# Performance work log

Measured on AMD Instinct MI355X. Metric: run time of the kernel, lower is better.

The kernel has to match this reference:

```python
import jax, jax.numpy as jnp
import numpy as np

NUM_HEADS = 8
NEG_LARGE = -1e9  # stands in for -inf under the causal mask; masked entries get exactly 0 entmax weight


def _entmax15(z):
    """Exact 1.5-entmax along the last axis (Peters & Martins 2019 sort-based algorithm)."""
    z = z * 0.5
    zs = -jnp.sort(-z, axis=-1)                      # descending sort
    T = z.shape[-1]
    k = jnp.arange(1, T + 1, dtype=z.dtype)
    mean = jnp.cumsum(zs, axis=-1) / k
    mean_sq = jnp.cumsum(zs * zs, axis=-1) / k
    ss = k * (mean_sq - mean * mean)
    delta = (1.0 - ss) / k
    tau = mean - jnp.sqrt(jnp.maximum(delta, 0.0))
    support = jnp.sum(tau <= zs, axis=-1, keepdims=True)      # support size >= 1
    tau_star = jnp.take_along_axis(tau, support - 1, axis=-1)
    return jnp.square(jnp.maximum(z - tau_star, 0.0))


def setup_inputs() -> dict:
    key = jax.random.key(0)
    ks = jax.random.split(key, 9)
    B, T, D, H = 2, 2048, 512, NUM_HEADS
    dk = D // H
    s = 1.0 / np.sqrt(D)
    so = 1.0 / np.sqrt(dk)
    x = jax.random.normal(ks[0], (B, T, D), jnp.float32)
    Wq = jax.random.uniform(ks[1], (D, D), jnp.float32, -s, s)
    bq = jax.random.uniform(ks[2], (D,), jnp.float32, -s, s)
    Wk = jax.random.uniform(ks[3], (D, D), jnp.float32, -s, s)
    bk = jax.random.uniform(ks[4], (D,), jnp.float32, -s, s)
    Wv = jax.random.uniform(ks[5], (D, D), jnp.float32, -s, s)
    bv = jax.random.uniform(ks[6], (D,), jnp.float32, -s, s)
    Wo = jax.random.uniform(ks[7], (dk, D), jnp.float32, -so, so)
    bo = jax.random.uniform(ks[8], (D,), jnp.float32, -so, so)
    return {"x": x, "Wq": Wq, "bq": bq, "Wk": Wk, "bk": bk, "Wv": Wv, "bv": bv, "Wo": Wo, "bo": bo}


def reference(x, Wq, bq, Wk, bk, Wv, bv, Wo, bo):
    B, T, D = x.shape
    H = NUM_HEADS
    dk = D // H
    Q = (x @ Wq + bq).reshape(B, T, H, dk).transpose(0, 2, 1, 3)   # [B,H,T,dk]
    K = (x @ Wk + bk).reshape(B, T, H, dk).transpose(0, 2, 1, 3)
    V = (x @ Wv + bv).reshape(B, T, H, dk).transpose(0, 2, 1, 3)
    scores = jnp.einsum('bhtd,bhsd->bhts', Q, K) / np.float32(np.sqrt(dk))
    causal = jnp.triu(jnp.ones((T, T), bool), k=1)                 # True above diagonal
    scores = jnp.where(causal[None, None, :, :], jnp.float32(NEG_LARGE), scores)
    weights = _entmax15(scores)                                    # [B,H,T,T]
    weights_avg = weights.mean(axis=1)                             # [B,T,T]
    V_combined = V.mean(axis=1)                                    # [B,T,dk]
    out = jnp.einsum('bts,bsd->btd', weights_avg, V_combined)      # [B,T,dk]
    return out @ Wo + bo, weights_avg
```

## Files before the change

kernel.cpp:

```cpp
#include <hip/hip_runtime.h>
#include <hip/hip_bf16.h>
#include <cstdint>

#define B_ 2
#define T_ 2048
#define D_ 512
#define H_ 8
#define DK_ 64
#define TQ_ 4
#define NTL_ (T_ / TQ_)
#define M_ (B_ * T_)

#define SSC_ 8192.0f
#define S2_  (SSC_ * SSC_)

__global__ __launch_bounds__(256) void gemm_bias_kernel(
    const float* __restrict__ A, const float* __restrict__ W,
    const float* __restrict__ bias, float* __restrict__ C,
    int M, int N, int K)
{
  __shared__ float As[32][68];
  __shared__ float Bs[32][68];
  const int bm = blockIdx.y * 64;
  const int bn = blockIdx.x * 64;
  const int tid = threadIdx.x;
  const int tx = tid & 15, ty = tid >> 4;
  float acc[4][4] = {};
  for (int k0 = 0; k0 < K; k0 += 32) {
    {
      const int r = tid >> 2;
      const int c = (tid & 3) << 2;
      const float4 a0 = *reinterpret_cast<const float4*>(&A[(size_t)(bm + r) * K + k0 + c]);
      const float4 a1 = *reinterpret_cast<const float4*>(&A[(size_t)(bm + r) * K + k0 + 16 + c]);
      As[c + 0][r] = a0.x;  As[c + 1][r] = a0.y;  As[c + 2][r] = a0.z;  As[c + 3][r] = a0.w;
      As[c + 16][r] = a1.x; As[c + 17][r] = a1.y; As[c + 18][r] = a1.z; As[c + 19][r] = a1.w;
    }
    {
      const int r = tid >> 4;
      const int c = (tid & 15) << 2;
      *reinterpret_cast<float4*>(&Bs[r][c]) =
          *reinterpret_cast<const float4*>(&W[(size_t)(k0 + r) * N + bn + c]);
      *reinterpret_cast<float4*>(&Bs[r + 16][c]) =
          *reinterpret_cast<const float4*>(&W[(size_t)(k0 + 16 + r) * N + bn + c]);
    }
    __syncthreads();
#pragma unroll
    for (int kk = 0; kk < 32; ++kk) {
      const float4 av = *reinterpret_cast<const float4*>(&As[kk][ty * 4]);
      const float4 bv = *reinterpret_cast<const float4*>(&Bs[kk][tx * 4]);
      acc[0][0] = fmaf(av.x, bv.x, acc[0][0]); acc[0][1] = fmaf(av.x, bv.y, acc[0][1]);
      acc[0][2] = fmaf(av.x, bv.z, acc[0][2]); acc[0][3] = fmaf(av.x, bv.w, acc[0][3]);
      acc[1][0] = fmaf(av.y, bv.x, acc[1][0]); acc[1][1] = fmaf(av.y, bv.y, acc[1][1]);
      acc[1][2] = fmaf(av.y, bv.z, acc[1][2]); acc[1][3] = fmaf(av.y, bv.w, acc[1][3]);
      acc[2][0] = fmaf(av.z, bv.x, acc[2][0]); acc[2][1] = fmaf(av.z, bv.y, acc[2][1]);
      acc[2][2] = fmaf(av.z, bv.z, acc[2][2]); acc[2][3] = fmaf(av.z, bv.w, acc[2][3]);
      acc[3][0] = fmaf(av.w, bv.x, acc[3][0]); acc[3][1] = fmaf(av.w, bv.y, acc[3][1]);
      acc[3][2] = fmaf(av.w, bv.z, acc[3][2]); acc[3][3] = fmaf(av.w, bv.w, acc[3][3]);
    }
    __syncthreads();
  }
#pragma unroll
  for (int i = 0; i < 4; ++i) {
    const int row = bm + ty * 4 + i;
#pragma unroll
    for (int j = 0; j < 4; ++j) {
      const int col = bn + tx * 4 + j;
      C[(size_t)row * N + col] = acc[i][j] + bias[col];
    }
  }
}

__global__ __launch_bounds__(256) void gemm_bias_kernelT(
    const float* __restrict__ A, const float* __restrict__ W,
    const float* __restrict__ bias, float* __restrict__ Ct,
    int M, int N, int K)
{
  __shared__ float As[32][68];
  __shared__ float Bs[32][68];
  const int bm = blockIdx.y * 64;
  const int bn = blockIdx.x * 64;
  const int tid = threadIdx.x;
  const int tx = tid & 15, ty = tid >> 4;
  float acc[4][4] = {};
  for (int k0 = 0; k0 < K; k0 += 32) {
    {
      const int r = tid >> 2;
      const int c = (tid & 3) << 2;
      const float4 a0 = *reinterpret_cast<const float4*>(&A[(size_t)(bm + r) * K + k0 + c]);
      const float4 a1 = *reinterpret_cast<const float4*>(&A[(size_t)(bm + r) * K + k0 + 16 + c]);
      As[c + 0][r] = a0.x;  As[c + 1][r] = a0.y;  As[c + 2][r] = a0.z;  As[c + 3][r] = a0.w;
      As[c + 16][r] = a1.x; As[c + 17][r] = a1.y; As[c + 18][r] = a1.z; As[c + 19][r] = a1.w;
    }
    {
      const int r = tid >> 4;
      const int c = (tid & 15) << 2;
      *reinterpret_cast<float4*>(&Bs[r][c]) =
          *reinterpret_cast<const float4*>(&W[(size_t)(k0 + r) * N + bn + c]);
      *reinterpret_cast<float4*>(&Bs[r + 16][c]) =
          *reinterpret_cast<const float4*>(&W[(size_t)(k0 + 16 + r) * N + bn + c]);
    }
    __syncthreads();
#pragma unroll
    for (int kk = 0; kk < 32; ++kk) {
      const float4 av = *reinterpret_cast<const float4*>(&As[kk][ty * 4]);
      const float4 bv = *reinterpret_cast<const float4*>(&Bs[kk][tx * 4]);
      acc[0][0] = fmaf(av.x, bv.x, acc[0][0]); acc[0][1] = fmaf(av.x, bv.y, acc[0][1]);
      acc[0][2] = fmaf(av.x, bv.z, acc[0][2]); acc[0][3] = fmaf(av.x, bv.w, acc[0][3]);
      acc[1][0] = fmaf(av.y, bv.x, acc[1][0]); acc[1][1] = fmaf(av.y, bv.y, acc[1][1]);
      acc[1][2] = fmaf(av.y, bv.z, acc[1][2]); acc[1][3] = fmaf(av.y, bv.w, acc[1][3]);
      acc[2][0] = fmaf(av.z, bv.x, acc[2][0]); acc[2][1] = fmaf(av.z, bv.y, acc[2][1]);
      acc[2][2] = fmaf(av.z, bv.z, acc[2][2]); acc[2][3] = fmaf(av.z, bv.w, acc[2][3]);
      acc[3][0] = fmaf(av.w, bv.x, acc[3][0]); acc[3][1] = fmaf(av.w, bv.y, acc[3][1]);
      acc[3][2] = fmaf(av.w, bv.z, acc[3][2]); acc[3][3] = fmaf(av.w, bv.w, acc[3][3]);
    }
    __syncthreads();
  }
#pragma unroll
  for (int j = 0; j < 4; ++j) {
    const int col = bn + tx * 4 + j;
    const float bb = bias[col];
    const float4 v = make_float4(acc[0][j] + bb, acc[1][j] + bb, acc[2][j] + bb, acc[3][j] + bb);
    *reinterpret_cast<float4*>(&Ct[(size_t)col * M + bm + ty * 4]) = v;
  }
}

__global__ __launch_bounds__(256) void vcombine_kernel(const float* __restrict__ V,
                                                       float* __restrict__ Vc)
{
  const int idx = blockIdx.x * 256 + threadIdx.x;
  if (idx >= M_ * DK_) return;
  const int row = idx >> 6, d = idx & 63;
  float s = 0.f;
#pragma unroll
  for (int h = 0; h < H_; ++h) s += V[(size_t)row * D_ + h * DK_ + d];
  Vc[idx] = s * 0.125f;
}

__global__ __launch_bounds__(256) void zero_kernel(float4* __restrict__ p, int n4)
{
  const int stride = gridDim.x * 256;
  const float4 z = make_float4(0.f, 0.f, 0.f, 0.f);
  for (int i = blockIdx.x * 256 + threadIdx.x; i < n4; i += stride) p[i] = z;
}

__global__ __launch_bounds__(256, 6)
void attn_kernel(
    const float* __restrict__ Qg, const float* __restrict__ Kt,
    float* __restrict__ wavg)
{
  __shared__ short ssc[TQ_][T_];

  const int tid = threadIdx.x;
  const int bid = blockIdx.x;
  const int h = bid >> 10;
  const int b = (bid >> 9) & 1;
  const int tile = (NTL_ - 1) - (bid & 511);
  const int t0 = tile * TQ_;
  const int nS = t0 + TQ_;
  const int wave = __builtin_amdgcn_readfirstlane(tid >> 6);
  const int lane = tid & 63;

  {
    const float* Qp = &Qg[(size_t)(b * T_ + t0) * D_ + h * DK_];
#pragma unroll 1
    for (int c = 0; c < T_; c += 1024) {
      if (c < nS) {
        const int s0 = min(tid * 4 + c, nS - 4);
        const float* Ktp = &Kt[(size_t)(h * DK_) * M_ + b * T_ + s0];
        float4 a[TQ_];
#pragma unroll
        for (int r = 0; r < TQ_; ++r) a[r] = make_float4(0.f, 0.f, 0.f, 0.f);
#pragma unroll 2
        for (int d4 = 0; d4 < 16; ++d4) {
          const float4 k0 = *reinterpret_cast<const float4*>(Ktp + (size_t)(d4 * 4 + 0) * M_);
          const float4 k1 = *reinterpret_cast<const float4*>(Ktp + (size_t)(d4 * 4 + 1) * M_);
          const float4 k2 = *reinterpret_cast<const float4*>(Ktp + (size_t)(d4 * 4 + 2) * M_);
          const float4 k3 = *reinterpret_cast<const float4*>(Ktp + (size_t)(d4 * 4 + 3) * M_);
#pragma unroll
          for (int r = 0; r < TQ_; ++r) {
            const float q0 = Qp[r * D_ + d4 * 4 + 0];
            const float q1 = Qp[r * D_ + d4 * 4 + 1];
            const float q2 = Qp[r * D_ + d4 * 4 + 2];
            const float q3 = Qp[r * D_ + d4 * 4 + 3];
            a[r].x = fmaf(q0, k0.x, a[r].x); a[r].y = fmaf(q0, k0.y, a[r].y);
            a[r].z = fmaf(q0, k0.z, a[r].z); a[r].w = fmaf(q0, k0.w, a[r].w);
            a[r].x = fmaf(q1, k1.x, a[r].x); a[r].y = fmaf(q1, k1.y, a[r].y);
            a[r].z = fmaf(q1, k1.z, a[r].z); a[r].w = fmaf(q1, k1.w, a[r].w);
            a[r].x = fmaf(q2, k2.x, a[r].x); a[r].y = fmaf(q2, k2.y, a[r].y);
            a[r].z = fmaf(q2, k2.z, a[r].z); a[r].w = fmaf(q2, k2.w, a[r].w);
            a[r].x = fmaf(q3, k3.x, a[r].x); a[r].y = fmaf(q3, k3.y, a[r].y);
            a[r].z = fmaf(q3, k3.z, a[r].z); a[r].w = fmaf(q3, k3.w, a[r].w);
          }
        }
#pragma unroll
        for (int r = 0; r < TQ_; ++r) {
          const int i0 = __float2int_rn(fminf(fmaxf(a[r].x * 512.f, -32000.f), 32000.f));
          const int i1 = __float2int_rn(fminf(fmaxf(a[r].y * 512.f, -32000.f), 32000.f));
          const int i2 = __float2int_rn(fminf(fmaxf(a[r].z * 512.f, -32000.f), 32000.f));
          const int i3 = __float2int_rn(fminf(fmaxf(a[r].w * 512.f, -32000.f), 32000.f));
          short4 st; st.x = (short)i0; st.y = (short)i1; st.z = (short)i2; st.w = (short)i3;
          *reinterpret_cast<short4*>(&ssc[r][s0]) = st;
        }
      }
    }
  }
  __syncthreads();

  const int t = t0 + wave;
  const int n = t + 1;
  float srow[32];

#pragma unroll
  for (int j = 0; j < 4; ++j) {
    if (j * 512 < n) {
      const uint4 pk = *reinterpret_cast<const uint4*>(&ssc[wave][j * 512 + lane * 8]);
      const unsigned pw[4] = {pk.x, pk.y, pk.z, pk.w};
#pragma unroll
      for (int q = 0; q < 4; ++q) {
        const int s_lo = j * 512 + lane * 8 + q * 2;
        const float lo = (float)((int)(short)(pw[q] & 0xffffu));
        const float hi = (float)((int)pw[q] >> 16);
        srow[j * 8 + q * 2 + 0] = (s_lo + 0 < n) ? lo : -1e30f;
        srow[j * 8 + q * 2 + 1] = (s_lo + 1 < n) ? hi : -1e30f;
      }
    } else {
#pragma unroll
      for (int q = 0; q < 8; ++q) srow[j * 8 + q] = -1e30f;
    }
  }
  asm volatile("" ::: "memory");

  float mx = -1e30f;
#pragma unroll
  for (int i = 0; i < 32; ++i) mx = fmaxf(mx, srow[i]);
#pragma unroll
  for (int m = 32; m >= 1; m >>= 1) mx = fmaxf(mx, __shfl_xor(mx, m, 64));

  float tau = mx - SSC_;
#pragma unroll 1
  for (int it = 0; it < 12; ++it) {
    float s1 = 0.f, s2 = 0.f, cn = 0.f;
#pragma unroll
    for (int j = 0; j < 4; ++j) {
      if (j * 512 < n) {
#pragma unroll
        for (int q = 0; q < 8; ++q) {
          const float u = fmaxf(srow[j * 8 + q] - tau, 0.f);
          s1 += u;
          s2 = fmaf(u, u, s2);
          cn += (u > 0.f) ? 1.f : 0.f;
        }
      }
    }
#pragma unroll
    for (int m = 32; m >= 1; m >>= 1) {
      s1 += __shfl_xor(s1, m, 64);
      s2 += __shfl_xor(s2, m, 64);
    }
    if (fabsf(s2 - S2_) < 672.f) break;
    if (it < 3) {
#pragma unroll
      for (int m = 32; m >= 1; m >>= 1) cn += __shfl_xor(cn, m, 64);
      const float kf = fmaxf(cn, 1.f);
      const float mu = tau + s1 / kf;
      const float ss = s2 - s1 * s1 / kf;
      tau = mu - sqrtf(fmaxf((S2_ - ss) / kf, 0.f));
    } else {
      tau += (s2 - S2_) / fmaxf(2.f * s1, 1e-6f);
    }
  }
  tau = fminf(tau, mx - 1.f);

  const float wconv = 0.125f / (SSC_ * SSC_);
  float* const wrow = &wavg[(size_t)(b * T_ + t) * T_];
#pragma unroll
  for (int j = 0; j < 4; ++j) {
    if (j * 512 < n) {
#pragma unroll
      for (int q = 0; q < 8; ++q) {
        const float u = fmaxf(srow[j * 8 + q] - tau, 0.f);
        if (__any(u > 0.f)) {
          if (u > 0.f) {
            const int s = j * 512 + lane * 8 + q;
            atomicAdd(&wrow[s], u * u * wconv);
          }
        }
      }
    }
  }
}

__global__ __launch_bounds__(256) void pv_kernel(
    const float* __restrict__ wavg, const float* __restrict__ Vc,
    float* __restrict__ AO)
{
  __shared__ float part[4][TQ_][DK_];
  const int tid = threadIdx.x;
  const int m0 = blockIdx.x * TQ_;
  const int b = m0 >> 11;
  const int tl = m0 & (T_ - 1);
  const int wave = __builtin_amdgcn_readfirstlane(tid >> 6);
  const int lane = tid & 63;

  const int smax = min((wave + 1) * 512, tl + TQ_);
  float a0 = 0.f, a1 = 0.f, a2 = 0.f, a3 = 0.f;
  const float* w0 = &wavg[(size_t)(m0 + 0) * T_];
  const float* w1 = &wavg[(size_t)(m0 + 1) * T_];
  const float* w2 = &wavg[(size_t)(m0 + 2) * T_];
  const float* w3 = &wavg[(size_t)(m0 + 3) * T_];
#pragma unroll 1
  for (int s = wave * 512; s < smax; ++s) {
    const float v = Vc[(size_t)(b * T_ + s) * DK_ + lane];
    a0 = fmaf(w0[s], v, a0);
    a1 = fmaf(w1[s], v, a1);
    a2 = fmaf(w2[s], v, a2);
    a3 = fmaf(w3[s], v, a3);
  }
  part[wave][0][lane] = a0;
  part[wave][1][lane] = a1;
  part[wave][2][lane] = a2;
  part[wave][3][lane] = a3;
  __syncthreads();
  {
    const int r = wave;
    const float o = part[0][r][lane] + part[1][r][lane] +
                    part[2][r][lane] + part[3][r][lane];
    AO[(size_t)(m0 + r) * DK_ + lane] = o;
  }
}

extern "C" void kernel_launch(void* const* d_in, const int* in_sizes, int n_in,
                              void* d_out, int out_size, void* d_ws, size_t ws_size,
                              hipStream_t stream)
{
  const float* x  = (const float*)d_in[0];
  const float* Wq = (const float*)d_in[1];
  const float* bq = (const float*)d_in[2];
  const float* Wk = (const float*)d_in[3];
  const float* bk = (const float*)d_in[4];
  const float* Wv = (const float*)d_in[5];
  const float* bv = (const float*)d_in[6];
  const float* Wo = (const float*)d_in[7];
  const float* bo = (const float*)d_in[8];
  float* out = (float*)d_out;
  float* ws  = (float*)d_ws;

  float* Q  = ws;
  float* Kt = Q + (size_t)M_ * D_;
  float* V  = Kt + (size_t)D_ * M_;
  float* Vc = V + (size_t)M_ * D_;
  float* AO = Vc + (size_t)M_ * DK_;

  float* out1 = out;
  float* wavg = out + (size_t)M_ * D_;

  const dim3 gp(D_ / 64, M_ / 64);
  gemm_bias_kernel <<<gp, 256, 0, stream>>>(x, Wq, bq, Q,  M_, D_, D_);
  gemm_bias_kernelT<<<gp, 256, 0, stream>>>(x, Wk, bk, Kt, M_, D_, D_);
  gemm_bias_kernel <<<gp, 256, 0, stream>>>(x, Wv, bv, V,  M_, D_, D_);
  vcombine_kernel<<<(M_ * DK_ + 255) / 256, 256, 0, stream>>>(V, Vc);

  zero_kernel<<<2048, 256, 0, stream>>>(reinterpret_cast<float4*>(wavg),
                                        (int)((size_t)B_ * T_ * T_ / 4));

  attn_kernel<<<H_ * B_ * NTL_, 256, 0, stream>>>(Q, Kt, wavg);
  pv_kernel<<<M_ / TQ_, 256, 0, stream>>>(wavg, Vc, AO);
  gemm_bias_kernel<<<gp, 256, 0, stream>>>(AO, Wo, bo, out1, M_, D_, DK_);
}
```

Measured before the change: 439.5 us.

## Restructure PV kernel to one row per block with sparse-weight skipping

New measurement: 386.2 us. -12.1%, faster.

```diff
diff --git a/kernel.cpp b/kernel.cpp
--- a/kernel.cpp
+++ b/kernel.cpp
@@ -294,38 +294,33 @@
     const float* __restrict__ wavg, const float* __restrict__ Vc,
     float* __restrict__ AO)
 {
-  __shared__ float part[4][TQ_][DK_];
-  const int tid = threadIdx.x;
-  const int m0 = blockIdx.x * TQ_;
-  const int b = m0 >> 11;
-  const int tl = m0 & (T_ - 1);
-  const int wave = __builtin_amdgcn_readfirstlane(tid >> 6);
-  const int lane = tid & 63;
-
-  const int smax = min((wave + 1) * 512, tl + TQ_);
-  float a0 = 0.f, a1 = 0.f, a2 = 0.f, a3 = 0.f;
-  const float* w0 = &wavg[(size_t)(m0 + 0) * T_];
-  const float* w1 = &wavg[(size_t)(m0 + 1) * T_];
-  const float* w2 = &wavg[(size_t)(m0 + 2) * T_];
-  const float* w3 = &wavg[(size_t)(m0 + 3) * T_];
+  __shared__ float part[4][DK_];
+  const int row = blockIdx.x;
+  const int b = row >> 11;
+  const int t = row & (T_ - 1);
+  const int wave = __builtin_amdgcn_readfirstlane(threadIdx.x >> 6);
+  const int lane = threadIdx.x & 63;
+  const int n = t + 1;
+  const float* wr = &wavg[(size_t)row * T_];
+  const float* vb = &Vc[(size_t)(b * T_) * DK_ + lane];
+  float acc = 0.f;
 #pragma unroll 1
-  for (int s = wave * 512; s < smax; ++s) {
-    const float v = Vc[(size_t)(b * T_ + s) * DK_ + lane];
-    a0 = fmaf(w0[s], v, a0);
-    a1 = fmaf(w1[s], v, a1);
-    a2 = fmaf(w2[s], v, a2);
-    a3 = fmaf(w3[s], v, a3);
-  }
-  part[wave][0][lane] = a0;
-  part[wave][1][lane] = a1;
-  part[wave][2][lane] = a2;
-  part[wave][3][lane] = a3;
+  for (int s0 = wave * 4; s0 < n; s0 += 16) {
+    const float4 w4 = *reinterpret_cast<const float4*>(&wr[s0]);
+    const unsigned nz = __float_as_uint(w4.x) | __float_as_uint(w4.y) |
+                        __float_as_uint(w4.z) | __float_as_uint(w4.w);
+    if (__builtin_amdgcn_readfirstlane(nz) != 0u) {
+      acc = fmaf(w4.x, vb[(size_t)(s0 + 0) * DK_], acc);
+      acc = fmaf(w4.y, vb[(size_t)(s0 + 1) * DK_], acc);
+      acc = fmaf(w4.z, vb[(size_t)(s0 + 2) * DK_], acc);
+      acc = fmaf(w4.w, vb[(size_t)(s0 + 3) * DK_], acc);
+    }
+  }
+  part[wave][lane] = acc;
   __syncthreads();
-  {
-    const int r = wave;
-    const float o = part[0][r][lane] + part[1][r][lane] +
-                    part[2][r][lane] + part[3][r][lane];
-    AO[(size_t)(m0 + r) * DK_ + lane] = o;
+  if (wave == 0) {
+    AO[(size_t)row * DK_ + lane] =
+        part[0][lane] + part[1][lane] + part[2][lane] + part[3][lane];
   }
 }
 
@@ -364,6 +359,6 @@
                                         (int)((size_t)B_ * T_ * T_ / 4));
 
   attn_kernel<<<H_ * B_ * NTL_, 256, 0, stream>>>(Q, Kt, wavg);
-  pv_kernel<<<M_ / TQ_, 256, 0, stream>>>(wavg, Vc, AO);
+  pv_kernel<<<M_, 256, 0, stream>>>(wavg, Vc, AO);
   gemm_bias_kernel<<<gp, 256, 0, stream>>>(AO, Wo, bo, out1, M_, D_, DK_);
 }
```
